# Kernel tuning notes

Hardware: AMD Instinct MI355X
Metric: run time of the kernel (lower is better)

Reference implementation:

```python
import jax, jax.numpy as jnp
import numpy as np

SIM_THR = 0.05
TEMPERATURE = 0.1
LAM = 0.5


def setup_inputs() -> dict:
    key = jax.random.key(0)
    k1, k2, k3 = jax.random.split(key, 3)
    N, D, DC, K = 4096, 512, 14, 336
    return {
        "features": jax.random.normal(k1, (N, D), dtype=jnp.float32),
        "continuous": jax.random.normal(k2, (N, DC), dtype=jnp.float32),
        "categorical": jax.random.uniform(k3, (N, K), dtype=jnp.float32),
        "len_categorical": 336,
    }


def _cdist(x):
    # pairwise euclidean distance, [N, N]
    sq = jnp.sum(x * x, axis=1)
    d2 = sq[:, None] + sq[None, :] - 2.0 * (x @ x.T)
    return jnp.sqrt(jnp.maximum(d2, 0.0))


def reference(features, continuous, categorical, len_categorical):
    N = features.shape[0]
    # similarity from continuous (rescaled to [-1, 1]) and categorical parts
    cont_sim = 1.0 / (1.0 + _cdist(continuous)) * 2.0 - 1.0
    cat_sim = (categorical @ categorical.T) / len_categorical
    similarity = LAM * cont_sim + (1.0 - LAM) * cat_sim
    # zero the diagonal
    eye = jnp.eye(N, dtype=similarity.dtype)
    similarity = similarity * (1.0 - eye)
    # per-row positive mask: within SIM_THR of the row max
    row_max = jnp.max(similarity, axis=1, keepdims=True)
    mask = (similarity >= row_max - SIM_THR).astype(features.dtype)
    # normalized feature logits
    f = features / jnp.linalg.norm(features, axis=1, keepdims=True)
    logits = (f @ f.T) / TEMPERATURE
    exp_sim = jnp.exp(logits)
    positives = jnp.sum(exp_sim * mask, axis=1)
    loss = -jnp.log(positives / jnp.sum(exp_sim, axis=1))
    return jnp.mean(loss)
```

## Files before the change

kernel.cpp:

```cpp
#include <hip/hip_runtime.h>
#include <math.h>

#define NN    4096
#define DCC   14
#define KCATN 336
#define KXP   416
#define DF    512
#define NT    32
#define NTRI  528
#define NCSIM 20
#define NCF   24

typedef __attribute__((ext_vector_type(4))) float f32x4;
typedef __attribute__((ext_vector_type(8))) short short8;
typedef unsigned short ushort_t;
typedef unsigned long long u64;

__device__ __forceinline__ f32x4 mfma16(short8 a, short8 b, f32x4 c) {
  return __builtin_amdgcn_mfma_f32_16x16x32_bf16(a, b, c, 0, 0, 0);
}
__device__ __forceinline__ ushort_t f2bf(float x) {
  unsigned u = __float_as_uint(x);
  return (ushort_t)((u + 0x7fffu + ((u >> 16) & 1u)) >> 16);
}
__device__ __forceinline__ float bf2f(ushort_t u) {
  return __uint_as_float(((unsigned)u) << 16);
}
__device__ __forceinline__ float sim_of(float cdot, float kdot, float si, float sj, float invl) {
  float d2 = fmaxf(si + sj - 2.f * cdot, 0.f);
  float cs = 1.0f / (1.0f + sqrtf(d2)) * 2.0f - 1.0f;
  return 0.5f * cs + 0.5f * (kdot * invl);
}

__device__ __forceinline__ void gload_lds16(const ushort_t* g, ushort_t* l) {
  __builtin_amdgcn_global_load_lds(
      (const __attribute__((address_space(1))) unsigned int*)g,
      (__attribute__((address_space(3))) unsigned int*)l, 16, 0, 0);
}

__device__ __forceinline__ void tile_map(int b, int* bip, int* bjp) {
  int t = (b & 7) * 66 + (b >> 3);
  int RI = 0, rem = t;
  for (; RI < 8; ++RI) {
    int rowcnt = 10 + 16 * (7 - RI);
    if (rem < rowcnt) break;
    rem -= rowcnt;
  }
  if (rem < 10) {
    int si = 0;
    while (rem >= 4 - si) { rem -= 4 - si; ++si; }
    *bip = RI * 4 + si; *bjp = RI * 4 + si + rem;
  } else {
    rem -= 10;
    int RJ = RI + 1 + (rem >> 4);
    int w = rem & 15;
    *bip = RI * 4 + (w >> 2); *bjp = RJ * 4 + (w & 3);
  }
}

__device__ __forceinline__ void stage_sim_chunk(
    int c, int i0b, int j0b,
    const ushort_t* __restrict__ xch, const ushort_t* __restrict__ xcl,
    ushort_t* Ab, ushort_t* Bb, int tid) {
  const int w = tid >> 6, lane = tid & 63;
  const int g = lane & 7, rsub = lane >> 3;
  const int gs = g ^ rsub;
  const ushort_t* srcA;
  const ushort_t* srcB;
  if (c == 0)      srcA = (gs < 4) ? xch + gs * 8 : xcl + (gs - 4) * 8;
  else if (c == 1) srcA = (gs < 4) ? xch + gs * 8 : xch + 384 + (gs - 4) * 8;
  else if (c < 8)  srcA = xch + 32 + (c - 2) * 64 + gs * 8;
  else if (c < 14) srcA = xcl + 32 + (c - 8) * 64 + gs * 8;
  else             srcA = xch + 32 + (c - 14) * 64 + gs * 8;
  if (c == 0)      srcB = (gs < 4) ? xch + gs * 8 : xch + (gs - 4) * 8;
  else if (c == 1) srcB = (gs < 4) ? xcl + gs * 8 : xch + 384 + (gs - 4) * 8;
  else if (c < 14) srcB = xch + 32 + ((c - 2) % 6) * 64 + gs * 8;
  else             srcB = xcl + 32 + (c - 14) * 64 + gs * 8;
  #pragma unroll
  for (int q = 0; q < 4; ++q) {
    const int row = (w * 4 + q) * 8 + rsub;
    gload_lds16(srcA + (size_t)(i0b + row) * KXP, Ab + (w * 4 + q) * 512);
    gload_lds16(srcB + (size_t)(j0b + row) * KXP, Bb + (w * 4 + q) * 512);
  }
}

__device__ __forceinline__ void stage_f_chunk(
    int c, int i0b, int j0b,
    const ushort_t* __restrict__ fhh, const ushort_t* __restrict__ fhl,
    ushort_t* Ab, ushort_t* Bb, int tid) {
  const int w = tid >> 6, lane = tid & 63;
  const int g = lane & 7, rsub = lane >> 3;
  const int gs = g ^ rsub;
  const ushort_t* baseA = (c < 8) ? fhh + c * 64 : (c < 16) ? fhl + (c - 8) * 64 : fhh + (c - 16) * 64;
  const ushort_t* baseB = (c < 16) ? fhh + (c & 7) * 64 : fhl + (c - 16) * 64;
  #pragma unroll
  for (int q = 0; q < 4; ++q) {
    const int row = (w * 4 + q) * 8 + rsub;
    gload_lds16(baseA + (size_t)(i0b + row) * DF + gs * 8, Ab + (w * 4 + q) * 512);
    gload_lds16(baseB + (size_t)(j0b + row) * DF + gs * 8, Bb + (w * 4 + q) * 512);
  }
}

__device__ __forceinline__ void compute_chunk(const ushort_t* Ab, const ushort_t* Bb,
                                              int wm, int wn, int l15, int lg,
                                              f32x4 acc[4][4]) {
  const int swz = l15 & 7;
  #pragma unroll
  for (int ks = 0; ks < 2; ++ks) {
    short8 a[4], b[4];
    const int gph = ((ks * 4 + lg) ^ swz) * 8;
    #pragma unroll
    for (int mf = 0; mf < 4; ++mf)
      a[mf] = *(const short8*)&Ab[(wm * 64 + mf * 16 + l15) * 64 + gph];
    #pragma unroll
    for (int nf = 0; nf < 4; ++nf)
      b[nf] = *(const short8*)&Bb[(wn * 64 + nf * 16 + l15) * 64 + gph];
    #pragma unroll
    for (int mf = 0; mf < 4; ++mf)
      #pragma unroll
      for (int nf = 0; nf < 4; ++nf)
        acc[mf][nf] = mfma16(a[mf], b[nf], acc[mf][nf]);
  }
}

__global__ __launch_bounds__(64) void prep_kernel(
    const float* __restrict__ feat, const float* __restrict__ cont,
    const float* __restrict__ cat,
    ushort_t* __restrict__ fhh, ushort_t* __restrict__ fhl,
    ushort_t* __restrict__ xch, ushort_t* __restrict__ xcl,
    float* __restrict__ csq, float* __restrict__ rm,
    float* __restrict__ pos, float* __restrict__ den) {
  int i = blockIdx.x;
  int t = threadIdx.x;

  float fv[8];
  float s = 0.f;
  #pragma unroll
  for (int r = 0; r < 8; ++r) { fv[r] = feat[i * DF + r * 64 + t]; s += fv[r] * fv[r]; }
  #pragma unroll
  for (int off = 32; off > 0; off >>= 1) s += __shfl_down(s, off);
  s = __shfl(s, 0);
  float inv = 1.0f / sqrtf(s);
  #pragma unroll
  for (int r = 0; r < 8; ++r) {
    float x = fv[r] * inv;
    ushort_t h = f2bf(x);
    fhh[i * DF + r * 64 + t] = h;
    fhl[i * DF + r * 64 + t] = f2bf(x - bf2f(h));
  }

  float cv = (t < DCC) ? cont[i * DCC + t] : 0.f;
  float cs = cv * cv;
  #pragma unroll
  for (int off = 32; off > 0; off >>= 1) cs += __shfl_down(cs, off);
  cs = __shfl(cs, 0);

  #pragma unroll
  for (int r = 0; r < 7; ++r) {
    int k = r * 64 + t;
    if (k < KXP) {
      float v = 0.f;
      if (k < DCC) v = cont[i * DCC + k];
      else if (k >= 32 && k < 32 + KCATN) v = cat[i * KCATN + (k - 32)];
      ushort_t h = f2bf(v);
      xch[i * KXP + k] = h;
      xcl[i * KXP + k] = f2bf(v - bf2f(h));
    }
  }

  if (t == 0) {
    csq[i] = cs;
    rm[i] = 0.f;
    pos[i] = 0.f;
    den[i] = 0.f;
  }
}

__global__ __launch_bounds__(256, 2) void simmax_kernel(
    const ushort_t* __restrict__ xch, const ushort_t* __restrict__ xcl,
    const float* __restrict__ csq, float* __restrict__ rm,
    float* __restrict__ simbuf, const int* __restrict__ lcp) {
  __shared__ ushort_t Ab[2][128 * 64];
  __shared__ ushort_t Bb[2][128 * 64];
  int bi, bj; tile_map(blockIdx.x, &bi, &bj);
  const int tid = threadIdx.x;
  const int lane = tid & 63, w = tid >> 6;
  const int wm = w >> 1, wn = w & 1;
  const int l15 = lane & 15, lg = lane >> 4;
  const int i0b = bi * 128, j0b = bj * 128;

  f32x4 accC[4][4], accK[4][4];
  #pragma unroll
  for (int a = 0; a < 4; ++a)
    #pragma unroll
    for (int b = 0; b < 4; ++b) { accC[a][b] = (f32x4){0.f,0.f,0.f,0.f}; accK[a][b] = (f32x4){0.f,0.f,0.f,0.f}; }

  stage_sim_chunk(0, i0b, j0b, xch, xcl, Ab[0], Bb[0], tid);
  __syncthreads();
  for (int c = 0; c < NCSIM; ++c) {
    if (c + 1 < NCSIM)
      stage_sim_chunk(c + 1, i0b, j0b, xch, xcl, Ab[(c + 1) & 1], Bb[(c + 1) & 1], tid);
    if (c < 2) compute_chunk(Ab[c & 1], Bb[c & 1], wm, wn, l15, lg, accC);
    else       compute_chunk(Ab[c & 1], Bb[c & 1], wm, wn, l15, lg, accK);
    __syncthreads();
  }

  const int i0 = i0b + wm * 64, j0 = j0b + wn * 64;
  const float invl = 1.0f / (float)(*lcp);
  float csqi[4][4], csqj[4];
  #pragma unroll
  for (int mf = 0; mf < 4; ++mf)
    #pragma unroll
    for (int r = 0; r < 4; ++r) csqi[mf][r] = csq[i0 + mf * 16 + lg * 4 + r];
  #pragma unroll
  for (int nf = 0; nf < 4; ++nf) csqj[nf] = csq[j0 + nf * 16 + l15];

  float rmaxr[4][4], cmax[4];
  #pragma unroll
  for (int mf = 0; mf < 4; ++mf)
    #pragma unroll
    for (int r = 0; r < 4; ++r) rmaxr[mf][r] = -1e30f;
  #pragma unroll
  for (int nf = 0; nf < 4; ++nf) cmax[nf] = -1e30f;

  #pragma unroll
  for (int mf = 0; mf < 4; ++mf)
    #pragma unroll
    for (int nf = 0; nf < 4; ++nf)
      #pragma unroll
      for (int r = 0; r < 4; ++r) {
        int gi = i0 + mf * 16 + lg * 4 + r;
        int gj = j0 + nf * 16 + l15;
        float sim = sim_of(accC[mf][nf][r], accK[mf][nf][r], csqi[mf][r], csqj[nf], invl);
        if (gi == gj) sim = 0.f;
        rmaxr[mf][r] = fmaxf(rmaxr[mf][r], sim);
        cmax[nf] = fmaxf(cmax[nf], sim);
        accC[mf][nf][r] = sim;
      }

  #pragma unroll
  for (int mf = 0; mf < 4; ++mf)
    #pragma unroll
    for (int r = 0; r < 4; ++r) {
      float v = rmaxr[mf][r];
      #pragma unroll
      for (int off = 1; off < 16; off <<= 1) v = fmaxf(v, __shfl_xor(v, off));
      if (l15 == 0) atomicMax((int*)&rm[i0 + mf * 16 + lg * 4 + r], __float_as_int(v));
    }
  if (bi != bj) {
    #pragma unroll
    for (int nf = 0; nf < 4; ++nf) {
      float v = cmax[nf];
      v = fmaxf(v, __shfl_xor(v, 16));
      v = fmaxf(v, __shfl_xor(v, 32));
      if (lg == 0) atomicMax((int*)&rm[j0 + nf * 16 + l15], __float_as_int(v));
    }
  }

  float* slot = simbuf + (size_t)blockIdx.x * 16384 + tid * 64;
  #pragma unroll
  for (int mf = 0; mf < 4; ++mf)
    #pragma unroll
    for (int nf = 0; nf < 4; ++nf)
      *(f32x4*)&slot[mf * 16 + nf * 4] = accC[mf][nf];
}

__global__ __launch_bounds__(256, 2) void loss_kernel(
    const ushort_t* __restrict__ fhh, const ushort_t* __restrict__ fhl,
    const float* __restrict__ rm, const float* __restrict__ simbuf,
    float* __restrict__ pos, float* __restrict__ den) {
  __shared__ ushort_t Ab[2][128 * 64];
  __shared__ ushort_t Bb[2][128 * 64];
  int bi, bj; tile_map(blockIdx.x, &bi, &bj);
  const int tid = threadIdx.x;
  const int lane = tid & 63, w = tid >> 6;
  const int wm = w >> 1, wn = w & 1;
  const int l15 = lane & 15, lg = lane >> 4;
  const int i0b = bi * 128, j0b = bj * 128;
  const int i0 = i0b + wm * 64, j0 = j0b + wn * 64;

  stage_f_chunk(0, i0b, j0b, fhh, fhl, Ab[0], Bb[0], tid);

  float rmi[4][4], rmj[4];
  #pragma unroll
  for (int mf = 0; mf < 4; ++mf)
    #pragma unroll
    for (int r = 0; r < 4; ++r) rmi[mf][r] = rm[i0 + mf * 16 + lg * 4 + r] - 0.05f;
  #pragma unroll
  for (int nf = 0; nf < 4; ++nf) rmj[nf] = rm[j0 + nf * 16 + l15] - 0.05f;

  const float* slot = simbuf + (size_t)blockIdx.x * 16384 + tid * 64;
  u64 mA = 0, mB = 0;
  #pragma unroll
  for (int mf = 0; mf < 4; ++mf)
    #pragma unroll
    for (int nf = 0; nf < 4; ++nf) {
      f32x4 sv = *(const f32x4*)&slot[mf * 16 + nf * 4];
      #pragma unroll
      for (int r = 0; r < 4; ++r) {
        u64 bit = 1ull << (mf * 16 + nf * 4 + r);
        if (sv[r] >= rmi[mf][r]) mA |= bit;
        if (sv[r] >= rmj[nf]) mB |= bit;
      }
    }

  __syncthreads();
  f32x4 facc[4][4];
  #pragma unroll
  for (int a = 0; a < 4; ++a)
    #pragma unroll
    for (int b = 0; b < 4; ++b) facc[a][b] = (f32x4){0.f,0.f,0.f,0.f};
  for (int c = 0; c < NCF; ++c) {
    if (c + 1 < NCF)
      stage_f_chunk(c + 1, i0b, j0b, fhh, fhl, Ab[(c + 1) & 1], Bb[(c + 1) & 1], tid);
    compute_chunk(Ab[c & 1], Bb[c & 1], wm, wn, l15, lg, facc);
    __syncthreads();
  }

  float posA[4][4], denA[4][4], posB[4], denB[4];
  #pragma unroll
  for (int mf = 0; mf < 4; ++mf)
    #pragma unroll
    for (int r = 0; r < 4; ++r) { posA[mf][r] = 0.f; denA[mf][r] = 0.f; }
  #pragma unroll
  for (int nf = 0; nf < 4; ++nf) { posB[nf] = 0.f; denB[nf] = 0.f; }

  #pragma unroll
  for (int mf = 0; mf < 4; ++mf)
    #pragma unroll
    for (int nf = 0; nf < 4; ++nf)
      #pragma unroll
      for (int r = 0; r < 4; ++r) {
        float e = __expf(facc[mf][nf][r] * 10.0f);
        denA[mf][r] += e;
        denB[nf] += e;
        u64 bit = 1ull << (mf * 16 + nf * 4 + r);
        if (mA & bit) posA[mf][r] += e;
        if (mB & bit) posB[nf] += e;
      }

  #pragma unroll
  for (int mf = 0; mf < 4; ++mf)
    #pragma unroll
    for (int r = 0; r < 4; ++r) {
      float p = posA[mf][r], d = denA[mf][r];
      #pragma unroll
      for (int off = 1; off < 16; off <<= 1) { p += __shfl_xor(p, off); d += __shfl_xor(d, off); }
      if (l15 == 0) {
        int gi = i0 + mf * 16 + lg * 4 + r;
        atomicAdd(&pos[gi], p);
        atomicAdd(&den[gi], d);
      }
    }
  if (bi != bj) {
    #pragma unroll
    for (int nf = 0; nf < 4; ++nf) {
      float p = posB[nf], d = denB[nf];
      p += __shfl_xor(p, 16); d += __shfl_xor(d, 16);
      p += __shfl_xor(p, 32); d += __shfl_xor(d, 32);
      if (lg == 0) {
        int gj = j0 + nf * 16 + l15;
        atomicAdd(&pos[gj], p);
        atomicAdd(&den[gj], d);
      }
    }
  }
}

__global__ __launch_bounds__(256) void reduce_kernel(const float* __restrict__ pos,
                                                     const float* __restrict__ den,
                                                     float* __restrict__ out) {
  __shared__ float sred[4];
  int t = threadIdx.x;
  float s = 0.f;
  for (int i = t; i < NN; i += 256) s += -logf(pos[i] / den[i]);
  #pragma unroll
  for (int off = 32; off > 0; off >>= 1) s += __shfl_down(s, off);
  if ((t & 63) == 0) sred[t >> 6] = s;
  __syncthreads();
  if (t == 0) out[0] = (sred[0] + sred[1] + sred[2] + sred[3]) * (1.0f / NN);
}

extern "C" void kernel_launch(void* const* d_in, const int* in_sizes, int n_in,
                              void* d_out, int out_size, void* d_ws, size_t ws_size,
                              hipStream_t stream) {
  (void)in_sizes; (void)n_in; (void)out_size; (void)ws_size;
  const float* feat = (const float*)d_in[0];
  const float* cont = (const float*)d_in[1];
  const float* cat  = (const float*)d_in[2];
  const int*   lc   = (const int*)d_in[3];
  float* out = (float*)d_out;

  ushort_t* fhh = (ushort_t*)d_ws;
  ushort_t* fhl = fhh + (size_t)NN * DF;
  ushort_t* xch = fhl + (size_t)NN * DF;
  ushort_t* xcl = xch + (size_t)NN * KXP;
  float* csq = (float*)(xcl + (size_t)NN * KXP);
  float* rm  = csq + NN;
  float* pos = rm + NN;
  float* den = pos + NN;
  float* simbuf = den + NN;

  prep_kernel<<<NN, 64, 0, stream>>>(feat, cont, cat, fhh, fhl, xch, xcl, csq, rm, pos, den);
  simmax_kernel<<<NTRI, 256, 0, stream>>>(xch, xcl, csq, rm, simbuf, lc);
  loss_kernel<<<NTRI, 256, 0, stream>>>(fhh, fhl, rm, simbuf, pos, den);
  reduce_kernel<<<1, 256, 0, stream>>>(pos, den, out);
}
```

Before: 222.5 us.

## Single-buffer LDS tiles and raise occupancy to four blocks per CU

Both GEMM-style kernels drop their double-buffered shared memory tiles in favour of a single buffer, adding an extra barrier so each chunk is loaded only after compute on the previous one has finished. Launch bounds go from 2 to 4 blocks per CU, so the hardware can hide latency by switching between more resident blocks instead of relying on in-block prefetch. The trade-off is that loads and MFMA no longer overlap inside a block, and the tighter register budget may cause spills, especially in simmax, which holds two 4x4 accumulator sets.

```diff
diff --git a/kernel.cpp b/kernel.cpp
--- a/kernel.cpp
+++ b/kernel.cpp
@@ -176,12 +176,12 @@
   }
 }
 
-__global__ __launch_bounds__(256, 2) void simmax_kernel(
+__global__ __launch_bounds__(256, 4) void simmax_kernel(
     const ushort_t* __restrict__ xch, const ushort_t* __restrict__ xcl,
     const float* __restrict__ csq, float* __restrict__ rm,
     float* __restrict__ simbuf, const int* __restrict__ lcp) {
-  __shared__ ushort_t Ab[2][128 * 64];
-  __shared__ ushort_t Bb[2][128 * 64];
+  __shared__ ushort_t Ab[128 * 64];
+  __shared__ ushort_t Bb[128 * 64];
   int bi, bj; tile_map(blockIdx.x, &bi, &bj);
   const int tid = threadIdx.x;
   const int lane = tid & 63, w = tid >> 6;
@@ -195,14 +195,16 @@
     #pragma unroll
     for (int b = 0; b < 4; ++b) { accC[a][b] = (f32x4){0.f,0.f,0.f,0.f}; accK[a][b] = (f32x4){0.f,0.f,0.f,0.f}; }
 
-  stage_sim_chunk(0, i0b, j0b, xch, xcl, Ab[0], Bb[0], tid);
+  stage_sim_chunk(0, i0b, j0b, xch, xcl, Ab, Bb, tid);
   __syncthreads();
   for (int c = 0; c < NCSIM; ++c) {
-    if (c + 1 < NCSIM)
-      stage_sim_chunk(c + 1, i0b, j0b, xch, xcl, Ab[(c + 1) & 1], Bb[(c + 1) & 1], tid);
-    if (c < 2) compute_chunk(Ab[c & 1], Bb[c & 1], wm, wn, l15, lg, accC);
-    else       compute_chunk(Ab[c & 1], Bb[c & 1], wm, wn, l15, lg, accK);
+    if (c < 2) compute_chunk(Ab, Bb, wm, wn, l15, lg, accC);
+    else       compute_chunk(Ab, Bb, wm, wn, l15, lg, accK);
     __syncthreads();
+    if (c + 1 < NCSIM) {
+      stage_sim_chunk(c + 1, i0b, j0b, xch, xcl, Ab, Bb, tid);
+      __syncthreads();
+    }
   }
 
   const int i0 = i0b + wm * 64, j0 = j0b + wn * 64;
@@ -265,12 +267,12 @@
       *(f32x4*)&slot[mf * 16 + nf * 4] = accC[mf][nf];
 }
 
-__global__ __launch_bounds__(256, 2) void loss_kernel(
+__global__ __launch_bounds__(256, 4) void loss_kernel(
     const ushort_t* __restrict__ fhh, const ushort_t* __restrict__ fhl,
     const float* __restrict__ rm, const float* __restrict__ simbuf,
     float* __restrict__ pos, float* __restrict__ den) {
-  __shared__ ushort_t Ab[2][128 * 64];
-  __shared__ ushort_t Bb[2][128 * 64];
+  __shared__ ushort_t Ab[128 * 64];
+  __shared__ ushort_t Bb[128 * 64];
   int bi, bj; tile_map(blockIdx.x, &bi, &bj);
   const int tid = threadIdx.x;
   const int lane = tid & 63, w = tid >> 6;
@@ -279,7 +281,7 @@
   const int i0b = bi * 128, j0b = bj * 128;
   const int i0 = i0b + wm * 64, j0 = j0b + wn * 64;
 
-  stage_f_chunk(0, i0b, j0b, fhh, fhl, Ab[0], Bb[0], tid);
+  stage_f_chunk(0, i0b, j0b, fhh, fhl, Ab, Bb, tid);
 
   float rmi[4][4], rmj[4];
   #pragma unroll
@@ -311,10 +313,12 @@
     #pragma unroll
     for (int b = 0; b < 4; ++b) facc[a][b] = (f32x4){0.f,0.f,0.f,0.f};
   for (int c = 0; c < NCF; ++c) {
-    if (c + 1 < NCF)
-      stage_f_chunk(c + 1, i0b, j0b, fhh, fhl, Ab[(c + 1) & 1], Bb[(c + 1) & 1], tid);
-    compute_chunk(Ab[c & 1], Bb[c & 1], wm, wn, l15, lg, facc);
+    compute_chunk(Ab, Bb, wm, wn, l15, lg, facc);
     __syncthreads();
+    if (c + 1 < NCF) {
+      stage_f_chunk(c + 1, i0b, j0b, fhh, fhl, Ab, Bb, tid);
+      __syncthreads();
+    }
   }
 
   float posA[4][4], denA[4][4], posB[4], denB[4];
```

Result: slower. 257.8 us (+15.8%).
